# Performance work log

Measured on AMD Instinct MI355X. Metric: run time of the kernel, lower is better.

## Reference

```python
import jax, jax.numpy as jnp
import numpy as np

K_NEIGHBORS = 16
NUM_PATCHES = 32
W_NORMAL = 1.0
W_SURFVAR = 1.0


def _knn_centered(points, k):
    """points: [B, N, 3] -> k nearest neighbors re-centered at each point, [B, N, k, 3].
    Distances are computed on stop_gradient(points) to match torch's .detach()."""
    pd = jax.lax.stop_gradient(points)
    # squared pairwise distances [B, N, N] (sqrt is monotone -> topk order identical)
    d2 = jnp.sum((pd[:, :, None, :] - pd[:, None, :, :]) ** 2, axis=-1)
    _, idx = jax.lax.top_k(-d2, k)  # smallest-k indices, [B, N, k]
    knn = jax.vmap(lambda pts, id_: pts[id_])(points, idx)  # [B, N, k, 3]
    return knn - points[:, :, None, :]


def _eig_props(knn):
    """knn: [B, N, k, 3] -> (normal [B,N,3] = eigvec of smallest eigval, eigvals [B,N,3] ascending)."""
    cov = jnp.einsum('bnki,bnkj->bnij', knn, knn)  # [B, N, 3, 3]
    w, v = jnp.linalg.eigh(cov)  # ascending eigenvalues, matches torch.symeig
    return v[..., :, 0], w


def setup_inputs() -> dict:
    key = jax.random.key(0)
    pointCloud = jax.random.normal(key, (4, 8192, 3), dtype=jnp.float32)
    return {"pointCloud": pointCloud}


def reference(pointCloud):
    B, N, _ = pointCloud.shape
    pp = N // NUM_PATCHES

    # global kNN / normals / surface variance
    knn_g = _knn_centered(pointCloud, K_NEIGHBORS)
    nrm_g, w_g = _eig_props(knn_g)

    # patchwise: each patch is an independent small point cloud -> fold patches into batch
    patch_pts = pointCloud.reshape(B * NUM_PATCHES, pp, 3)
    knn_p = _knn_centered(patch_pts, K_NEIGHBORS)
    nrm_p, w_p = _eig_props(knn_p)
    nrm_p = nrm_p.reshape(B, N, 3)

    # normal loss (abs variant, sign-ambiguity-free)
    loss_n = jnp.mean(jnp.linalg.norm(jnp.abs(nrm_p) - jnp.abs(nrm_g), axis=2)) * W_NORMAL

    # surface variance loss: lambda_min / sum(lambda)
    sv_g = w_g[..., 0] / jnp.sum(w_g, axis=-1)            # [B, N]
    sv_p = (w_p[..., 0] / jnp.sum(w_p, axis=-1)).reshape(B, N)
    loss_sv = jnp.mean((sv_p - sv_g) ** 2) * W_SURFVAR

    return jnp.stack([loss_n, loss_sv])  # [2] (original returns list of two [1] tensors)
```

## Files before the change

### kernel.cpp

```cpp
#include <hip/hip_runtime.h>
#include <math.h>

#define KNN 16
#define NPTS 8192
#define PTCH 256
#define NPATCH 32
#define NBATCH 4
#define NQ 32
#define SSTRIDE 130
#define LAMBDA_T 64.0f

#define NC 16
#define NCELLS (NC * NC * NC)
#define GMIN -4.2f
#define ICS 1.9047619f

__device__ __forceinline__ float lam_f(float r, float s)
{
    const float C     = 0.063493636f;
    const float SQ2PI = 2.5066283f;
    const float IS2   = 0.70710678f;
    float a = fabsf(r - s), b = r + s;
    float amr = a - r;
    float coefA = amr * amr + 2.f - s * s;
    float I = 2.f * __expf(-0.5f * b * b) - coefA * __expf(-0.5f * a * a)
            + r * SQ2PI * (erff(b * IS2) - erff(a * IS2));
    float M = C * (3.14159265f / r) * I;
    if (s > r) {
        float u = s - r;
        M += 12.566371f * C * (1.2533141f * erff(u * IS2) - u * __expf(-0.5f * u * u));
    }
    return (float)NPTS * M;
}

__device__ __forceinline__ void jrot(double& app, double& aqq, double& apq,
                                     double& arp, double& arq,
                                     double& vp0, double& vq0,
                                     double& vp1, double& vq1,
                                     double& vp2, double& vq2)
{
    double g = apq;
    if (g == 0.0) return;
    double theta = (aqq - app) / (2.0 * g);
    double at = fabs(theta);
    double t = (at > 1.0e154) ? (0.5 / theta)
                              : (copysign(1.0, theta) / (at + sqrt(theta * theta + 1.0)));
    double c = 1.0 / sqrt(t * t + 1.0);
    double s = t * c;
    double tau = s / (1.0 + c);
    app -= t * g;
    aqq += t * g;
    apq = 0.0;
    double rp = arp, rq = arq;
    arp = rp - s * (rq + tau * rp);
    arq = rq + s * (rp - tau * rq);
    double p0 = vp0, q0 = vq0;
    vp0 = p0 - s * (q0 + tau * p0); vq0 = q0 + s * (p0 - tau * q0);
    double p1 = vp1, q1 = vq1;
    vp1 = p1 - s * (q1 + tau * p1); vq1 = q1 + s * (p1 - tau * q1);
    double p2 = vp2, q2 = vq2;
    vp2 = p2 - s * (q2 + tau * p2); vq2 = q2 + s * (p2 - tau * q2);
}

__device__ __forceinline__ void eig3(double a00, double a11, double a22,
                                     double a01, double a02, double a12,
                                     double& nx, double& ny, double& nz,
                                     double& lmin, double& lsum)
{
    double v00 = 1, v01 = 0, v02 = 0;
    double v10 = 0, v11 = 1, v12 = 0;
    double v20 = 0, v21 = 0, v22 = 1;
    double scale = fabs(a00) + fabs(a11) + fabs(a22) + fabs(a01) + fabs(a02) + fabs(a12);
    if (scale > 0.0) {
        for (int sweep = 0; sweep < 6; ++sweep) {
            double off = fabs(a01) + fabs(a02) + fabs(a12);
            if (off <= scale * 1e-15) break;
            jrot(a00, a11, a01, a02, a12, v00, v01, v10, v11, v20, v21);
            jrot(a00, a22, a02, a01, a12, v00, v02, v10, v12, v20, v22);
            jrot(a11, a22, a12, a01, a02, v01, v02, v11, v12, v21, v22);
        }
    }
    lsum = a00 + a11 + a22;
    lmin = a00; nx = v00; ny = v10; nz = v20;
    if (a11 < lmin) { lmin = a11; nx = v01; ny = v11; nz = v21; }
    if (a22 < lmin) { lmin = a22; nx = v02; ny = v12; nz = v22; }
}

__device__ __forceinline__ unsigned mkkey(float d2, unsigned idx) {
    return (__float_as_uint(d2) & 0xFFFFE000u) | idx;
}

__device__ __forceinline__ void insert16(unsigned key, unsigned* L)
{
    L[KNN - 1] = key;
    #pragma unroll
    for (int m = KNN - 1; m >= 1; --m) {
        unsigned a = L[m - 1], b = L[m];
        L[m - 1] = min(a, b);
        L[m]     = max(a, b);
    }
}

__device__ __forceinline__ void merge4(unsigned* L, int lane)
{
    #pragma unroll
    for (int step = 1; step <= 2; step <<= 1) {
        unsigned tmp[KNN];
        #pragma unroll
        for (int m = 0; m < KNN; ++m) tmp[m] = __shfl(L[m], lane ^ step, 64);
        for (int m = 0; m < KNN; ++m) {
            if (tmp[m] >= L[KNN - 1]) break;
            insert16(tmp[m], L);
        }
    }
}

__device__ __forceinline__ float rfl(float x) {
    return __int_as_float(__builtin_amdgcn_readfirstlane(__float_as_int(x)));
}
__device__ __forceinline__ unsigned mbcnt64(unsigned long long m) {
    return __builtin_amdgcn_mbcnt_hi((unsigned)(m >> 32),
           __builtin_amdgcn_mbcnt_lo((unsigned)m, 0u));
}

__device__ __forceinline__ int cidx(float v) {
    int i = (int)floorf((v - GMIN) * ICS);
    return min(max(i, 0), NC - 1);
}
__device__ __forceinline__ int cellOf(float x, float y, float z) {
    return (cidx(z) * NC + cidx(y)) * NC + cidx(x);
}

#define BT 1024
__global__ void __launch_bounds__(1024)
build_kernel(const float* __restrict__ pts, float* __restrict__ out,
             unsigned* __restrict__ cellStart, float4* __restrict__ sorted)
{
    __shared__ unsigned hist[NCELLS];
    __shared__ unsigned part[BT];
    const int b = blockIdx.x;
    const int t = threadIdx.x;
    if (b == 0 && t == 0) { out[0] = 0.0f; out[1] = 0.0f; }
    for (int i = t; i < NCELLS; i += BT) hist[i] = 0u;
    __syncthreads();
    const float* base = pts + (size_t)b * (NPTS * 3);
    float px[8], py[8], pz[8];
    int pc[8];
    #pragma unroll
    for (int k = 0; k < 8; ++k) {
        int i = k * BT + t;
        px[k] = base[i * 3 + 0];
        py[k] = base[i * 3 + 1];
        pz[k] = base[i * 3 + 2];
        pc[k] = cellOf(px[k], py[k], pz[k]);
        atomicAdd(&hist[pc[k]], 1u);
    }
    __syncthreads();
    unsigned loc[4], s = 0;
    #pragma unroll
    for (int i = 0; i < 4; ++i) { loc[i] = s; s += hist[t * 4 + i]; }
    part[t] = s;
    __syncthreads();
    for (int o = 1; o < BT; o <<= 1) {
        unsigned u = (t >= o) ? part[t - o] : 0u;
        __syncthreads();
        part[t] += u;
        __syncthreads();
    }
    unsigned basex = part[t] - s;
    unsigned* csb = cellStart + b * (NCELLS + 1);
    #pragma unroll
    for (int i = 0; i < 4; ++i) {
        unsigned e = basex + loc[i];
        csb[t * 4 + i] = e;
        hist[t * 4 + i] = e;
    }
    if (t == BT - 1) csb[NCELLS] = basex + s;
    __syncthreads();
    float4* sb = sorted + (size_t)b * NPTS;
    #pragma unroll
    for (int k = 0; k < 8; ++k) {
        int i = k * BT + t;
        unsigned slot = atomicAdd(&hist[pc[k]], 1u);
        float4 v;
        v.x = px[k]; v.y = py[k]; v.z = pz[k]; v.w = __uint_as_float((unsigned)i);
        sb[slot] = v;
    }
}

__global__ void __launch_bounds__(256, 4)
spl_main(const float* __restrict__ pts, float* __restrict__ out,
         const unsigned* __restrict__ cellStart, const float4* __restrict__ sortedp)
{
    __shared__ float4 pbuf4[PTCH];
    __shared__ unsigned survk[NQ * SSTRIDE];
    __shared__ unsigned cnts[NQ];
    __shared__ float gbuf[NQ];
    __shared__ double xbuf[NQ * 4];
    __shared__ double rb[4];

    const int t = threadIdx.x;
    const int w = t >> 6;
    const int lane = t & 63;
    const int p = blockIdx.x;
    const int eighth = blockIdx.y;
    const int b = blockIdx.z;

    const float* base = pts + (size_t)b * (NPTS * 3);
    const int qbase = p * PTCH + eighth * NQ;
    const unsigned* cs = cellStart + b * (NCELLS + 1);
    const float4* sp = sortedp + (size_t)b * NPTS;

    {
        const float* src = base + p * (PTCH * 3);
        float* dst = (float*)pbuf4;
        #pragma unroll
        for (int s = 0; s < 3; ++s) {
            int f = t + s * 256;
            int j = f / 3;
            int c = f - 3 * j;
            dst[j * 4 + c] = src[f];
        }
    }
    if (t < NQ) {
        int qi = qbase + t;
        float x = base[qi * 3 + 0], y = base[qi * 3 + 1], z = base[qi * 3 + 2];
        float r = fmaxf(sqrtf(x * x + y * y + z * z), 0.01f);
        float lo = 0.f, hi = 12.f;
        #pragma unroll 1
        for (int it = 0; it < 16; ++it) {
            float mid = 0.5f * (lo + hi);
            if (lam_f(r, mid) < LAMBDA_T) lo = mid; else hi = mid;
        }
        gbuf[t] = hi * hi;
    }
    __syncthreads();

    #pragma unroll 1
    for (int u = 0; u < 8; ++u) {
        const int q = w * 8 + u;
        float4 qv = pbuf4[eighth * NQ + q];
        float qx = rfl(qv.x), qy = rfl(qv.y), qz = rfl(qv.z);
        float g2 = rfl(gbuf[q]);
        float g = sqrtf(g2);
        int ixlo = cidx(qx - g), ixhi = cidx(qx + g);
        int iylo = cidx(qy - g), iyhi = cidx(qy + g);
        int izlo = cidx(qz - g), izhi = cidx(qz + g);
        int nx = ixhi - ixlo + 1;
        int ny = iyhi - iylo + 1;
        int nyz = ny * (izhi - izlo + 1);
        const int lR  = (nyz >= 8) ? 3 : (nyz >= 4) ? 2 : (nyz >= 2) ? 1 : 0;
        const int R   = 1 << lR;
        const int lsl = 6 - lR;
        const unsigned SL = 64u >> lR;
        const unsigned slot = (unsigned)lane & (SL - 1u);
        unsigned cnt = 0;
        unsigned sbase = (unsigned)q * SSTRIDE;
        #pragma unroll 1
        for (int r0 = 0; r0 < nyz; r0 += 64) {
            int r = r0 + lane;
            unsigned pk = 0;
            if (r < nyz) {
                int iz = izlo + r / ny;
                int iy = iylo + (r - (r / ny) * ny);
                int cb = (iz * NC + iy) * NC + ixlo;
                unsigned sB = cs[cb];
                pk = sB | ((cs[cb + nx] - sB) << 14);
            }
            int rmax = min(nyz - r0, 64);
            int gcount = (rmax + R - 1) >> lR;
            #pragma unroll 1
            for (int gg = 0; gg < gcount; ++gg) {
                unsigned pkm = __shfl(pk, (gg << lR) + (lane >> lsl), 64);
                unsigned sBm = pkm & 0x3FFFu;
                unsigned lm  = pkm >> 14;
                #pragma unroll 1
                for (unsigned st = slot; ; st += SL) {
                    bool in = st < lm;
                    if (!__any(in ? 1 : 0)) break;
                    float4 c = sp[min(sBm + st, (unsigned)(NPTS - 1))];
                    float dx = qx - c.x, dy = qy - c.y, dz = qz - c.z;
                    float d2 = dx * dx + dy * dy + dz * dz;
                    bool pass = in && (d2 < g2);
                    unsigned long long m = __ballot(pass);
                    if (pass) {
                        unsigned sw = min(cnt + mbcnt64(m), (unsigned)(SSTRIDE - 1));
                        survk[sbase + sw] = mkkey(d2, __float_as_uint(c.w));
                    }
                    cnt += (unsigned)__popcll(m);
                }
            }
        }
        if (lane == 0) cnts[q] = cnt;
    }
    __syncthreads();

    const int qq = lane >> 2;
    const int h = lane & 3;
    const int myq = (w & 1) * 16 + qq;
    float4 qv = pbuf4[eighth * NQ + myq];
    const float pqx = qv.x, pqy = qv.y, pqz = qv.z;

    double ngx = 0, ngy = 0, ngz = 0, svg = 0;

    if (w < 2) {
        unsigned gl[KNN];
        #pragma unroll
        for (int m = 0; m < KNN; ++m) gl[m] = 0xFFFFFFFFu;
        unsigned cnt = cnts[myq];
        bool valid = (cnt >= KNN) && (cnt <= SSTRIDE);
        if (valid) {
            unsigned share = (cnt + 3) >> 2;
            unsigned m0 = h * share;
            unsigned m1 = min(m0 + share, cnt);
            #pragma unroll 1
            for (unsigned m = m0; m < m1; ++m) {
                unsigned k = survk[myq * SSTRIDE + m];
                if (k < gl[KNN - 1]) insert16(k, gl);
            }
        }
        merge4(gl, lane);
        if (valid) {
            float g = gbuf[myq];
            float upper = __uint_as_float((gl[KNN - 1] & 0xFFFFE000u) + 0x2000u);
            valid = (upper < g * 0.999f - 1e-5f);
        }
        if (__any((h == 0 && !valid) ? 1 : 0)) {
            if (h == 0 && !valid) {
                #pragma unroll
                for (int m = 0; m < KNN; ++m) gl[m] = 0xFFFFFFFFu;
                #pragma unroll 1
                for (int i = 0; i < NPTS; ++i) {
                    float cx = base[i * 3 + 0];
                    float cy = base[i * 3 + 1];
                    float cz = base[i * 3 + 2];
                    float dx = pqx - cx, dy = pqy - cy, dz = pqz - cz;
                    float d2 = dx * dx + dy * dy + dz * dz;
                    unsigned k = mkkey(d2, (unsigned)i);
                    if (k < gl[KNN - 1]) insert16(k, gl);
                }
            }
        }
        if (h == 0) {
            double c00 = 0, c11 = 0, c22 = 0, c01 = 0, c02 = 0, c12 = 0;
            const double qxd = pqx, qyd = pqy, qzd = pqz;
            #pragma unroll
            for (int m = 0; m < KNN; ++m) {
                int idx = (int)(gl[m] & 0x1FFFu);
                double dx = (double)base[idx * 3 + 0] - qxd;
                double dy = (double)base[idx * 3 + 1] - qyd;
                double dz = (double)base[idx * 3 + 2] - qzd;
                c00 += dx * dx; c11 += dy * dy; c22 += dz * dz;
                c01 += dx * dy; c02 += dx * dz; c12 += dy * dz;
            }
            double lmin, lsum;
            eig3(c00, c11, c22, c01, c02, c12, ngx, ngy, ngz, lmin, lsum);
            svg = lmin / lsum;
        }
    } else {
        unsigned pl[KNN];
        #pragma unroll
        for (int m = 0; m < KNN; ++m) pl[m] = 0xFFFFFFFFu;
        const int j0 = h * 64;
        #pragma unroll 1
        for (int j = j0; j < j0 + 64; ++j) {
            float4 c = pbuf4[j];
            float dx = pqx - c.x, dy = pqy - c.y, dz = pqz - c.z;
            float d2 = dx * dx + dy * dy + dz * dz;
            unsigned k = mkkey(d2, (unsigned)j);
            if (k < pl[KNN - 1]) insert16(k, pl);
        }
        merge4(pl, lane);
        if (h == 0) {
            double c00 = 0, c11 = 0, c22 = 0, c01 = 0, c02 = 0, c12 = 0;
            const double qxd = pqx, qyd = pqy, qzd = pqz;
            #pragma unroll
            for (int m = 0; m < KNN; ++m) {
                int idx = (int)(pl[m] & 0x1FFFu);
                float4 cpt = pbuf4[idx];
                double dx = (double)cpt.x - qxd;
                double dy = (double)cpt.y - qyd;
                double dz = (double)cpt.z - qzd;
                c00 += dx * dx; c11 += dy * dy; c22 += dz * dz;
                c01 += dx * dy; c02 += dx * dz; c12 += dy * dz;
            }
            double nx, ny, nz, lmin, lsum;
            eig3(c00, c11, c22, c01, c02, c12, nx, ny, nz, lmin, lsum);
            xbuf[myq * 4 + 0] = nx;
            xbuf[myq * 4 + 1] = ny;
            xbuf[myq * 4 + 2] = nz;
            xbuf[myq * 4 + 3] = lmin / lsum;
        }
    }
    __syncthreads();

    double ln = 0.0, lsv = 0.0;
    if (w < 2 && h == 0) {
        double npx = xbuf[myq * 4 + 0];
        double npy = xbuf[myq * 4 + 1];
        double npz = xbuf[myq * 4 + 2];
        double svp = xbuf[myq * 4 + 3];
        double dx = fabs(npx) - fabs(ngx);
        double dy = fabs(npy) - fabs(ngy);
        double dz = fabs(npz) - fabs(ngz);
        ln  = sqrt(dx * dx + dy * dy + dz * dz);
        double ds = svp - svg;
        lsv = ds * ds;
    }
    if (w < 2) {
        #pragma unroll
        for (int o = 32; o > 0; o >>= 1) {
            ln  += __shfl_down(ln, o);
            lsv += __shfl_down(lsv, o);
        }
        if (lane == 0) { rb[w * 2 + 0] = ln; rb[w * 2 + 1] = lsv; }
    }
    __syncthreads();
    if (t == 0) {
        const double inv = 1.0 / (double)(NBATCH * NPTS);
        atomicAdd(&out[0], (float)((rb[0] + rb[2]) * inv));
        atomicAdd(&out[1], (float)((rb[1] + rb[3]) * inv));
    }
}

extern "C" void kernel_launch(void* const* d_in, const int* in_sizes, int n_in,
                              void* d_out, int out_size, void* d_ws, size_t ws_size,
                              hipStream_t stream)
{
    const float* pts = (const float*)d_in[0];
    float* out = (float*)d_out;

    unsigned char* ws = (unsigned char*)d_ws;
    unsigned* cellStart = (unsigned*)(ws);
    float4*   sorted    = (float4*)  (ws + 65552);

    hipLaunchKernelGGL(build_kernel, dim3(NBATCH), dim3(BT), 0, stream,
                       pts, out, cellStart, sorted);
    dim3 grid(NPATCH, 8, NBATCH);
    hipLaunchKernelGGL(spl_main, grid, dim3(256), 0, stream, pts, out, cellStart, sorted);
}
```

Measured before the change: 163.3 us.

## Split fused kNN kernel into gate, filter and select stages via workspace

```diff
diff --git a/kernel.cpp b/kernel.cpp
--- a/kernel.cpp
+++ b/kernel.cpp
@@ -185,6 +185,265 @@
         float4 v;
         v.x = px[k]; v.y = py[k]; v.z = pz[k]; v.w = __uint_as_float((unsigned)i);
         sb[slot] = v;
+    }
+}
+
+__global__ void __launch_bounds__(256)
+gate_kernel(const float* __restrict__ pts, float* __restrict__ g2buf)
+{
+    int q = blockIdx.x * 256 + threadIdx.x;
+    int b = q >> 13, i = q & (NPTS - 1);
+    const float* pp = pts + (size_t)b * (NPTS * 3) + (size_t)i * 3;
+    float x = pp[0], y = pp[1], z = pp[2];
+    float r = fmaxf(sqrtf(x * x + y * y + z * z), 0.01f);
+    float lo = 0.f, hi = 12.f;
+    #pragma unroll 1
+    for (int it = 0; it < 16; ++it) {
+        float mid = 0.5f * (lo + hi);
+        if (lam_f(r, mid) < LAMBDA_T) lo = mid; else hi = mid;
+    }
+    g2buf[q] = hi * hi;
+}
+
+__global__ void __launch_bounds__(256)
+filter_kernel(const float* __restrict__ pts, const float* __restrict__ g2buf,
+              const unsigned* __restrict__ cellStart,
+              const float4* __restrict__ sortedp,
+              unsigned* __restrict__ survk, unsigned* __restrict__ cnts)
+{
+    const int lane = threadIdx.x & 63;
+    const int wq = __builtin_amdgcn_readfirstlane(
+        (int)((blockIdx.x * 256u + (unsigned)threadIdx.x) >> 6));
+    const int b  = wq >> 13;
+    const int qi = wq & (NPTS - 1);
+    const float* base = pts + (size_t)b * (NPTS * 3);
+    const unsigned* cs = cellStart + b * (NCELLS + 1);
+    const float4* sp = sortedp + (size_t)b * NPTS;
+
+    const float qx = base[qi * 3 + 0];
+    const float qy = base[qi * 3 + 1];
+    const float qz = base[qi * 3 + 2];
+    const float g2 = g2buf[wq];
+    const float g  = sqrtf(g2);
+
+    int ixlo = cidx(qx - g), ixhi = cidx(qx + g);
+    int iylo = cidx(qy - g), iyhi = cidx(qy + g);
+    int izlo = cidx(qz - g), izhi = cidx(qz + g);
+    int nx = ixhi - ixlo + 1;
+    int ny = iyhi - iylo + 1;
+    int nyz = ny * (izhi - izlo + 1);
+    const int lR  = (nyz >= 8) ? 3 : (nyz >= 4) ? 2 : (nyz >= 2) ? 1 : 0;
+    const int R   = 1 << lR;
+    const int lsl = 6 - lR;
+    const unsigned SL = 64u >> lR;
+    const unsigned slot = (unsigned)lane & (SL - 1u);
+    unsigned cnt = 0;
+    unsigned sbase = (unsigned)wq * SSTRIDE;
+    #pragma unroll 1
+    for (int r0 = 0; r0 < nyz; r0 += 64) {
+        int r = r0 + lane;
+        unsigned pk = 0;
+        if (r < nyz) {
+            int iz = izlo + r / ny;
+            int iy = iylo + (r - (r / ny) * ny);
+            int cb = (iz * NC + iy) * NC + ixlo;
+            unsigned sB = cs[cb];
+            pk = sB | ((cs[cb + nx] - sB) << 14);
+        }
+        int rmax = min(nyz - r0, 64);
+        int gcount = (rmax + R - 1) >> lR;
+        #pragma unroll 1
+        for (int gg = 0; gg < gcount; ++gg) {
+            unsigned pkm = __shfl(pk, (gg << lR) + (lane >> lsl), 64);
+            unsigned sBm = pkm & 0x3FFFu;
+            unsigned lm  = pkm >> 14;
+            #pragma unroll 1
+            for (unsigned st = slot; ; st += SL) {
+                bool in = st < lm;
+                if (!__any(in ? 1 : 0)) break;
+                float4 c = sp[min(sBm + st, (unsigned)(NPTS - 1))];
+                float dx = qx - c.x, dy = qy - c.y, dz = qz - c.z;
+                float d2 = dx * dx + dy * dy + dz * dz;
+                bool pass = in && (d2 < g2);
+                unsigned long long m = __ballot(pass);
+                if (pass) {
+                    unsigned sw = min(cnt + mbcnt64(m), (unsigned)(SSTRIDE - 1));
+                    survk[sbase + sw] = mkkey(d2, __float_as_uint(c.w));
+                }
+                cnt += (unsigned)__popcll(m);
+            }
+        }
+    }
+    if (lane == 0) cnts[wq] = cnt;
+}
+
+__global__ void __launch_bounds__(256, 4)
+select_kernel(const float* __restrict__ pts, float* __restrict__ out,
+              const float* __restrict__ g2buf,
+              const unsigned* __restrict__ survk_g,
+              const unsigned* __restrict__ cnts_g)
+{
+    __shared__ float4 pbuf4[PTCH];
+    __shared__ unsigned survl[NQ * SSTRIDE];
+    __shared__ unsigned cnts[NQ];
+    __shared__ double xbuf[NQ * 4];
+    __shared__ double rb[4];
+
+    const int t = threadIdx.x;
+    const int w = t >> 6;
+    const int lane = t & 63;
+    const int p = blockIdx.x;
+    const int eighth = blockIdx.y;
+    const int b = blockIdx.z;
+
+    const float* base = pts + (size_t)b * (NPTS * 3);
+    const int qbase = p * PTCH + eighth * NQ;
+    const int qg0 = b * NPTS + qbase;
+
+    {
+        const float* src = base + p * (PTCH * 3);
+        float* dst = (float*)pbuf4;
+        #pragma unroll
+        for (int s = 0; s < 3; ++s) {
+            int f = t + s * 256;
+            int j = f / 3;
+            int c = f - 3 * j;
+            dst[j * 4 + c] = src[f];
+        }
+    }
+    {
+        const unsigned* src = survk_g + (size_t)qg0 * SSTRIDE;
+        #pragma unroll 1
+        for (int i = t; i < NQ * SSTRIDE; i += 256) survl[i] = src[i];
+        if (t < NQ) cnts[t] = cnts_g[qg0 + t];
+    }
+    __syncthreads();
+
+    const int qq = lane >> 2;
+    const int h = lane & 3;
+    const int myq = (w & 1) * 16 + qq;
+    float4 qv = pbuf4[eighth * NQ + myq];
+    const float pqx = qv.x, pqy = qv.y, pqz = qv.z;
+
+    double ngx = 0, ngy = 0, ngz = 0, svg = 0;
+
+    if (w < 2) {
+        unsigned gl[KNN];
+        #pragma unroll
+        for (int m = 0; m < KNN; ++m) gl[m] = 0xFFFFFFFFu;
+        unsigned cnt = cnts[myq];
+        bool valid = (cnt >= KNN) && (cnt <= SSTRIDE);
+        if (valid) {
+            unsigned share = (cnt + 3) >> 2;
+            unsigned m0 = h * share;
+            unsigned m1 = min(m0 + share, cnt);
+            #pragma unroll 1
+            for (unsigned m = m0; m < m1; ++m) {
+                unsigned k = survl[myq * SSTRIDE + m];
+                if (k < gl[KNN - 1]) insert16(k, gl);
+            }
+        }
+        merge4(gl, lane);
+        if (valid) {
+            float g = g2buf[qg0 + myq];
+            float upper = __uint_as_float((gl[KNN - 1] & 0xFFFFE000u) + 0x2000u);
+            valid = (upper < g * 0.999f - 1e-5f);
+        }
+        if (__any((h == 0 && !valid) ? 1 : 0)) {
+            if (h == 0 && !valid) {
+                #pragma unroll
+                for (int m = 0; m < KNN; ++m) gl[m] = 0xFFFFFFFFu;
+                #pragma unroll 1
+                for (int i = 0; i < NPTS; ++i) {
+                    float cx = base[i * 3 + 0];
+                    float cy = base[i * 3 + 1];
+                    float cz = base[i * 3 + 2];
+                    float dx = pqx - cx, dy = pqy - cy, dz = pqz - cz;
+                    float d2 = dx * dx + dy * dy + dz * dz;
+                    unsigned k = mkkey(d2, (unsigned)i);
+                    if (k < gl[KNN - 1]) insert16(k, gl);
+                }
+            }
+        }
+        if (h == 0) {
+            double c00 = 0, c11 = 0, c22 = 0, c01 = 0, c02 = 0, c12 = 0;
+            const double qxd = pqx, qyd = pqy, qzd = pqz;
+            #pragma unroll
+            for (int m = 0; m < KNN; ++m) {
+                int idx = (int)(gl[m] & 0x1FFFu);
+                double dx = (double)base[idx * 3 + 0] - qxd;
+                double dy = (double)base[idx * 3 + 1] - qyd;
+                double dz = (double)base[idx * 3 + 2] - qzd;
+                c00 += dx * dx; c11 += dy * dy; c22 += dz * dz;
+                c01 += dx * dy; c02 += dx * dz; c12 += dy * dz;
+            }
+            double lmin, lsum;
+            eig3(c00, c11, c22, c01, c02, c12, ngx, ngy, ngz, lmin, lsum);
+            svg = lmin / lsum;
+        }
+    } else {
+        unsigned pl[KNN];
+        #pragma unroll
+        for (int m = 0; m < KNN; ++m) pl[m] = 0xFFFFFFFFu;
+        const int j0 = h * 64;
+        #pragma unroll 1
+        for (int j = j0; j < j0 + 64; ++j) {
+            float4 c = pbuf4[j];
+            float dx = pqx - c.x, dy = pqy - c.y, dz = pqz - c.z;
+            float d2 = dx * dx + dy * dy + dz * dz;
+            unsigned k = mkkey(d2, (unsigned)j);
+            if (k < pl[KNN - 1]) insert16(k, pl);
+        }
+        merge4(pl, lane);
+        if (h == 0) {
+            double c00 = 0, c11 = 0, c22 = 0, c01 = 0, c02 = 0, c12 = 0;
+            const double qxd = pqx, qyd = pqy, qzd = pqz;
+            #pragma unroll
+            for (int m = 0; m < KNN; ++m) {
+                int idx = (int)(pl[m] & 0x1FFFu);
+                float4 cpt = pbuf4[idx];
+                double dx = (double)cpt.x - qxd;
+                double dy = (double)cpt.y - qyd;
+                double dz = (double)cpt.z - qzd;
+                c00 += dx * dx; c11 += dy * dy; c22 += dz * dz;
+                c01 += dx * dy; c02 += dx * dz; c12 += dy * dz;
+            }
+            double nx, ny, nz, lmin, lsum;
+            eig3(c00, c11, c22, c01, c02, c12, nx, ny, nz, lmin, lsum);
+            xbuf[myq * 4 + 0] = nx;
+            xbuf[myq * 4 + 1] = ny;
+            xbuf[myq * 4 + 2] = nz;
+            xbuf[myq * 4 + 3] = lmin / lsum;
+        }
+    }
+    __syncthreads();
+
+    double ln = 0.0, lsv = 0.0;
+    if (w < 2 && h == 0) {
+        double npx = xbuf[myq * 4 + 0];
+        double npy = xbuf[myq * 4 + 1];
+        double npz = xbuf[myq * 4 + 2];
+        double svp = xbuf[myq * 4 + 3];
+        double dx = fabs(npx) - fabs(ngx);
+        double dy = fabs(npy) - fabs(ngy);
+        double dz = fabs(npz) - fabs(ngz);
+        ln  = sqrt(dx * dx + dy * dy + dz * dz);
+        double ds = svp - svg;
+        lsv = ds * ds;
+    }
+    if (w < 2) {
+        #pragma unroll
+        for (int o = 32; o > 0; o >>= 1) {
+            ln  += __shfl_down(ln, o);
+            lsv += __shfl_down(lsv, o);
+        }
+        if (lane == 0) { rb[w * 2 + 0] = ln; rb[w * 2 + 1] = lsv; }
+    }
+    __syncthreads();
+    if (t == 0) {
+        const double inv = 1.0 / (double)(NBATCH * NPTS);
+        atomicAdd(&out[0], (float)((rb[0] + rb[2]) * inv));
+        atomicAdd(&out[1], (float)((rb[1] + rb[3]) * inv));
     }
 }
 
@@ -433,9 +692,23 @@
     unsigned char* ws = (unsigned char*)d_ws;
     unsigned* cellStart = (unsigned*)(ws);
     float4*   sorted    = (float4*)  (ws + 65552);
+    float*    g2buf     = (float*)   (ws + 589840);
+    unsigned* cnts      = (unsigned*)(ws + 720912);
+    unsigned* survk     = (unsigned*)(ws + 851984);
 
     hipLaunchKernelGGL(build_kernel, dim3(NBATCH), dim3(BT), 0, stream,
                        pts, out, cellStart, sorted);
-    dim3 grid(NPATCH, 8, NBATCH);
-    hipLaunchKernelGGL(spl_main, grid, dim3(256), 0, stream, pts, out, cellStart, sorted);
-}
+    if (ws_size >= (size_t)17891344) {
+        hipLaunchKernelGGL(gate_kernel, dim3(NBATCH * NPTS / 256), dim3(256), 0, stream,
+                           pts, g2buf);
+        hipLaunchKernelGGL(filter_kernel, dim3(NBATCH * NPTS / 4), dim3(256), 0, stream,
+                           pts, g2buf, cellStart, sorted, survk, cnts);
+        dim3 grid(NPATCH, 8, NBATCH);
+        hipLaunchKernelGGL(select_kernel, grid, dim3(256), 0, stream,
+                           pts, out, g2buf, survk, cnts);
+    } else {
+        dim3 grid(NPATCH, 8, NBATCH);
+        hipLaunchKernelGGL(spl_main, grid, dim3(256), 0, stream,
+                           pts, out, cellStart, sorted);
+    }
+}
```

Result: no change. 162.1 us (-0.7%).

## Split fused kNN kernel into gate, select, patch-select, eigen and reduce stages

Applied to the files above, without the earlier changes.

```diff
diff --git a/kernel.cpp b/kernel.cpp
--- a/kernel.cpp
+++ b/kernel.cpp
@@ -6,7 +6,6 @@
 #define PTCH 256
 #define NPATCH 32
 #define NBATCH 4
-#define NQ 32
 #define SSTRIDE 130
 #define LAMBDA_T 64.0f
 
@@ -115,9 +114,6 @@
     }
 }
 
-__device__ __forceinline__ float rfl(float x) {
-    return __int_as_float(__builtin_amdgcn_readfirstlane(__float_as_int(x)));
-}
 __device__ __forceinline__ unsigned mbcnt64(unsigned long long m) {
     return __builtin_amdgcn_mbcnt_hi((unsigned)(m >> 32),
            __builtin_amdgcn_mbcnt_lo((unsigned)m, 0u));
@@ -188,28 +184,159 @@
     }
 }
 
-__global__ void __launch_bounds__(256, 4)
-spl_main(const float* __restrict__ pts, float* __restrict__ out,
-         const unsigned* __restrict__ cellStart, const float4* __restrict__ sortedp)
+__global__ void __launch_bounds__(256)
+gate_kernel(const float* __restrict__ pts, float* __restrict__ g2buf)
+{
+    int q = blockIdx.x * 256 + threadIdx.x;
+    int b = q >> 13, i = q & (NPTS - 1);
+    const float* pp = pts + (size_t)b * (NPTS * 3) + (size_t)i * 3;
+    float x = pp[0], y = pp[1], z = pp[2];
+    float r = fmaxf(sqrtf(x * x + y * y + z * z), 0.01f);
+    float lo = 0.f, hi = 12.f;
+    #pragma unroll 1
+    for (int it = 0; it < 16; ++it) {
+        float mid = 0.5f * (lo + hi);
+        if (lam_f(r, mid) < LAMBDA_T) lo = mid; else hi = mid;
+    }
+    g2buf[q] = hi * hi;
+}
+
+__global__ void __launch_bounds__(256)
+fselect_kernel(const float* __restrict__ pts, const float* __restrict__ g2buf,
+               const unsigned* __restrict__ cellStart,
+               const float4* __restrict__ sortedp,
+               unsigned* __restrict__ idx16)
+{
+    __shared__ unsigned survl[4 * SSTRIDE];
+    const int t = threadIdx.x;
+    const int wv = t >> 6;
+    const int lane = t & 63;
+    const int wq = __builtin_amdgcn_readfirstlane(blockIdx.x * 4 + wv);
+    const int b  = wq >> 13;
+    const int qi = wq & (NPTS - 1);
+    const float* base = pts + (size_t)b * (NPTS * 3);
+    const unsigned* cs = cellStart + b * (NCELLS + 1);
+    const float4* sp = sortedp + (size_t)b * NPTS;
+    unsigned* sl = survl + wv * SSTRIDE;
+
+    const float qx = base[qi * 3 + 0];
+    const float qy = base[qi * 3 + 1];
+    const float qz = base[qi * 3 + 2];
+    const float g2 = g2buf[wq];
+    const float g  = sqrtf(g2);
+
+    int ixlo = cidx(qx - g), ixhi = cidx(qx + g);
+    int iylo = cidx(qy - g), iyhi = cidx(qy + g);
+    int izlo = cidx(qz - g), izhi = cidx(qz + g);
+    int nx = ixhi - ixlo + 1;
+    int ny = iyhi - iylo + 1;
+    int nyz = ny * (izhi - izlo + 1);
+    const int lR  = (nyz >= 8) ? 3 : (nyz >= 4) ? 2 : (nyz >= 2) ? 1 : 0;
+    const int R   = 1 << lR;
+    const int lsl = 6 - lR;
+    const unsigned SL = 64u >> lR;
+    const unsigned slot = (unsigned)lane & (SL - 1u);
+    unsigned cnt = 0;
+    #pragma unroll 1
+    for (int r0 = 0; r0 < nyz; r0 += 64) {
+        int r = r0 + lane;
+        unsigned pk = 0;
+        if (r < nyz) {
+            int iz = izlo + r / ny;
+            int iy = iylo + (r - (r / ny) * ny);
+            int cb = (iz * NC + iy) * NC + ixlo;
+            unsigned sB = cs[cb];
+            pk = sB | ((cs[cb + nx] - sB) << 14);
+        }
+        int rmax = min(nyz - r0, 64);
+        int gcount = (rmax + R - 1) >> lR;
+        #pragma unroll 1
+        for (int gg = 0; gg < gcount; ++gg) {
+            unsigned pkm = __shfl(pk, (gg << lR) + (lane >> lsl), 64);
+            unsigned sBm = pkm & 0x3FFFu;
+            unsigned lm  = pkm >> 14;
+            #pragma unroll 1
+            for (unsigned st = slot; ; st += SL) {
+                bool in = st < lm;
+                if (!__any(in ? 1 : 0)) break;
+                float4 c = sp[min(sBm + st, (unsigned)(NPTS - 1))];
+                float dx = qx - c.x, dy = qy - c.y, dz = qz - c.z;
+                float d2 = dx * dx + dy * dy + dz * dz;
+                bool pass = in && (d2 < g2);
+                unsigned long long m = __ballot(pass);
+                if (pass) {
+                    unsigned sw = min(cnt + mbcnt64(m), (unsigned)(SSTRIDE - 1));
+                    sl[sw] = mkkey(d2, __float_as_uint(c.w));
+                }
+                cnt += (unsigned)__popcll(m);
+            }
+        }
+    }
+
+    bool valid = (cnt >= KNN) && (cnt <= 128u);
+    if (valid) {
+        unsigned k0 = (lane < (int)cnt)      ? sl[lane]      : 0xFFFFFFFFu;
+        unsigned k1 = (lane + 64 < (int)cnt) ? sl[lane + 64] : 0xFFFFFFFFu;
+        unsigned P = 0;
+        #pragma unroll 1
+        for (int bit = 31; bit >= 0; --bit) {
+            unsigned mid = P | (1u << bit);
+            unsigned c = (unsigned)__popcll(__ballot(k0 < mid))
+                       + (unsigned)__popcll(__ballot(k1 < mid));
+            if (c < 16u) P = mid;
+        }
+        float upper = __uint_as_float((P & 0xFFFFE000u) + 0x2000u);
+        valid = (upper < g2 * 0.999f - 1e-5f);
+        if (valid) {
+            bool sel0 = (k0 <= P);
+            bool sel1 = (k1 <= P);
+            unsigned long long m0 = __ballot(sel0);
+            unsigned long long m1 = __ballot(sel1);
+            unsigned base1 = (unsigned)__popcll(m0);
+            if (sel0) sl[mbcnt64(m0)] = k0;
+            if (sel1) sl[base1 + mbcnt64(m1)] = k1;
+            unsigned myk = sl[lane & 15];
+            unsigned rnk = 0;
+            #pragma unroll
+            for (int j = 0; j < 16; ++j) {
+                unsigned kj = __shfl(myk, j, 64);
+                rnk += (kj < myk) ? 1u : 0u;
+            }
+            if (lane < 16)
+                idx16[(size_t)wq * 32 + rnk] = myk & 0x1FFFu;
+        }
+    }
+    if (!valid && lane == 0) {
+        unsigned gl[KNN];
+        #pragma unroll
+        for (int m = 0; m < KNN; ++m) gl[m] = 0xFFFFFFFFu;
+        #pragma unroll 1
+        for (int i = 0; i < NPTS; ++i) {
+            float cx = base[i * 3 + 0];
+            float cy = base[i * 3 + 1];
+            float cz = base[i * 3 + 2];
+            float dx = qx - cx, dy = qy - cy, dz = qz - cz;
+            float d2 = dx * dx + dy * dy + dz * dz;
+            unsigned k = mkkey(d2, (unsigned)i);
+            if (k < gl[KNN - 1]) insert16(k, gl);
+        }
+        unsigned* dst = idx16 + (size_t)wq * 32;
+        #pragma unroll
+        for (int m = 0; m < KNN; ++m) dst[m] = gl[m] & 0x1FFFu;
+    }
+}
+
+__global__ void __launch_bounds__(256)
+pselect_kernel(const float* __restrict__ pts, unsigned* __restrict__ idx16)
 {
     __shared__ float4 pbuf4[PTCH];
-    __shared__ unsigned survk[NQ * SSTRIDE];
-    __shared__ unsigned cnts[NQ];
-    __shared__ float gbuf[NQ];
-    __shared__ double xbuf[NQ * 4];
-    __shared__ double rb[4];
-
     const int t = threadIdx.x;
     const int w = t >> 6;
     const int lane = t & 63;
     const int p = blockIdx.x;
-    const int eighth = blockIdx.y;
+    const int quarter = blockIdx.y;
     const int b = blockIdx.z;
-
     const float* base = pts + (size_t)b * (NPTS * 3);
-    const int qbase = p * PTCH + eighth * NQ;
-    const unsigned* cs = cellStart + b * (NCELLS + 1);
-    const float4* sp = sortedp + (size_t)b * NPTS;
 
     {
         const float* src = base + p * (PTCH * 3);
@@ -222,204 +349,114 @@
             dst[j * 4 + c] = src[f];
         }
     }
-    if (t < NQ) {
-        int qi = qbase + t;
-        float x = base[qi * 3 + 0], y = base[qi * 3 + 1], z = base[qi * 3 + 2];
-        float r = fmaxf(sqrtf(x * x + y * y + z * z), 0.01f);
-        float lo = 0.f, hi = 12.f;
-        #pragma unroll 1
-        for (int it = 0; it < 16; ++it) {
-            float mid = 0.5f * (lo + hi);
-            if (lam_f(r, mid) < LAMBDA_T) lo = mid; else hi = mid;
-        }
-        gbuf[t] = hi * hi;
-    }
-    __syncthreads();
-
-    #pragma unroll 1
-    for (int u = 0; u < 8; ++u) {
-        const int q = w * 8 + u;
-        float4 qv = pbuf4[eighth * NQ + q];
-        float qx = rfl(qv.x), qy = rfl(qv.y), qz = rfl(qv.z);
-        float g2 = rfl(gbuf[q]);
-        float g = sqrtf(g2);
-        int ixlo = cidx(qx - g), ixhi = cidx(qx + g);
-        int iylo = cidx(qy - g), iyhi = cidx(qy + g);
-        int izlo = cidx(qz - g), izhi = cidx(qz + g);
-        int nx = ixhi - ixlo + 1;
-        int ny = iyhi - iylo + 1;
-        int nyz = ny * (izhi - izlo + 1);
-        const int lR  = (nyz >= 8) ? 3 : (nyz >= 4) ? 2 : (nyz >= 2) ? 1 : 0;
-        const int R   = 1 << lR;
-        const int lsl = 6 - lR;
-        const unsigned SL = 64u >> lR;
-        const unsigned slot = (unsigned)lane & (SL - 1u);
-        unsigned cnt = 0;
-        unsigned sbase = (unsigned)q * SSTRIDE;
-        #pragma unroll 1
-        for (int r0 = 0; r0 < nyz; r0 += 64) {
-            int r = r0 + lane;
-            unsigned pk = 0;
-            if (r < nyz) {
-                int iz = izlo + r / ny;
-                int iy = iylo + (r - (r / ny) * ny);
-                int cb = (iz * NC + iy) * NC + ixlo;
-                unsigned sB = cs[cb];
-                pk = sB | ((cs[cb + nx] - sB) << 14);
-            }
-            int rmax = min(nyz - r0, 64);
-            int gcount = (rmax + R - 1) >> lR;
-            #pragma unroll 1
-            for (int gg = 0; gg < gcount; ++gg) {
-                unsigned pkm = __shfl(pk, (gg << lR) + (lane >> lsl), 64);
-                unsigned sBm = pkm & 0x3FFFu;
-                unsigned lm  = pkm >> 14;
-                #pragma unroll 1
-                for (unsigned st = slot; ; st += SL) {
-                    bool in = st < lm;
-                    if (!__any(in ? 1 : 0)) break;
-                    float4 c = sp[min(sBm + st, (unsigned)(NPTS - 1))];
-                    float dx = qx - c.x, dy = qy - c.y, dz = qz - c.z;
-                    float d2 = dx * dx + dy * dy + dz * dz;
-                    bool pass = in && (d2 < g2);
-                    unsigned long long m = __ballot(pass);
-                    if (pass) {
-                        unsigned sw = min(cnt + mbcnt64(m), (unsigned)(SSTRIDE - 1));
-                        survk[sbase + sw] = mkkey(d2, __float_as_uint(c.w));
-                    }
-                    cnt += (unsigned)__popcll(m);
-                }
-            }
-        }
-        if (lane == 0) cnts[q] = cnt;
-    }
     __syncthreads();
 
     const int qq = lane >> 2;
     const int h = lane & 3;
-    const int myq = (w & 1) * 16 + qq;
-    float4 qv = pbuf4[eighth * NQ + myq];
+    const int qlocal = quarter * 64 + w * 16 + qq;
+    float4 qv = pbuf4[qlocal];
     const float pqx = qv.x, pqy = qv.y, pqz = qv.z;
 
-    double ngx = 0, ngy = 0, ngz = 0, svg = 0;
-
-    if (w < 2) {
-        unsigned gl[KNN];
+    unsigned pl[KNN];
+    #pragma unroll
+    for (int m = 0; m < KNN; ++m) pl[m] = 0xFFFFFFFFu;
+    const int j0 = h * 64;
+    #pragma unroll 4
+    for (int j = j0; j < j0 + 64; ++j) {
+        float4 c = pbuf4[j];
+        float dx = pqx - c.x, dy = pqy - c.y, dz = pqz - c.z;
+        float d2 = dx * dx + dy * dy + dz * dz;
+        unsigned k = mkkey(d2, (unsigned)j);
+        if (k < pl[KNN - 1]) insert16(k, pl);
+    }
+    merge4(pl, lane);
+    if (h == 0) {
+        int qid = b * NPTS + p * PTCH + qlocal;
+        unsigned* dst = idx16 + (size_t)qid * 32 + 16;
         #pragma unroll
-        for (int m = 0; m < KNN; ++m) gl[m] = 0xFFFFFFFFu;
-        unsigned cnt = cnts[myq];
-        bool valid = (cnt >= KNN) && (cnt <= SSTRIDE);
-        if (valid) {
-            unsigned share = (cnt + 3) >> 2;
-            unsigned m0 = h * share;
-            unsigned m1 = min(m0 + share, cnt);
-            #pragma unroll 1
-            for (unsigned m = m0; m < m1; ++m) {
-                unsigned k = survk[myq * SSTRIDE + m];
-                if (k < gl[KNN - 1]) insert16(k, gl);
-            }
-        }
-        merge4(gl, lane);
-        if (valid) {
-            float g = gbuf[myq];
-            float upper = __uint_as_float((gl[KNN - 1] & 0xFFFFE000u) + 0x2000u);
-            valid = (upper < g * 0.999f - 1e-5f);
-        }
-        if (__any((h == 0 && !valid) ? 1 : 0)) {
-            if (h == 0 && !valid) {
-                #pragma unroll
-                for (int m = 0; m < KNN; ++m) gl[m] = 0xFFFFFFFFu;
-                #pragma unroll 1
-                for (int i = 0; i < NPTS; ++i) {
-                    float cx = base[i * 3 + 0];
-                    float cy = base[i * 3 + 1];
-                    float cz = base[i * 3 + 2];
-                    float dx = pqx - cx, dy = pqy - cy, dz = pqz - cz;
-                    float d2 = dx * dx + dy * dy + dz * dz;
-                    unsigned k = mkkey(d2, (unsigned)i);
-                    if (k < gl[KNN - 1]) insert16(k, gl);
-                }
-            }
-        }
-        if (h == 0) {
-            double c00 = 0, c11 = 0, c22 = 0, c01 = 0, c02 = 0, c12 = 0;
-            const double qxd = pqx, qyd = pqy, qzd = pqz;
-            #pragma unroll
-            for (int m = 0; m < KNN; ++m) {
-                int idx = (int)(gl[m] & 0x1FFFu);
-                double dx = (double)base[idx * 3 + 0] - qxd;
-                double dy = (double)base[idx * 3 + 1] - qyd;
-                double dz = (double)base[idx * 3 + 2] - qzd;
-                c00 += dx * dx; c11 += dy * dy; c22 += dz * dz;
-                c01 += dx * dy; c02 += dx * dz; c12 += dy * dz;
-            }
-            double lmin, lsum;
-            eig3(c00, c11, c22, c01, c02, c12, ngx, ngy, ngz, lmin, lsum);
-            svg = lmin / lsum;
-        }
-    } else {
-        unsigned pl[KNN];
-        #pragma unroll
-        for (int m = 0; m < KNN; ++m) pl[m] = 0xFFFFFFFFu;
-        const int j0 = h * 64;
-        #pragma unroll 1
-        for (int j = j0; j < j0 + 64; ++j) {
-            float4 c = pbuf4[j];
-            float dx = pqx - c.x, dy = pqy - c.y, dz = pqz - c.z;
-            float d2 = dx * dx + dy * dy + dz * dz;
-            unsigned k = mkkey(d2, (unsigned)j);
-            if (k < pl[KNN - 1]) insert16(k, pl);
-        }
-        merge4(pl, lane);
-        if (h == 0) {
-            double c00 = 0, c11 = 0, c22 = 0, c01 = 0, c02 = 0, c12 = 0;
-            const double qxd = pqx, qyd = pqy, qzd = pqz;
-            #pragma unroll
-            for (int m = 0; m < KNN; ++m) {
-                int idx = (int)(pl[m] & 0x1FFFu);
-                float4 cpt = pbuf4[idx];
-                double dx = (double)cpt.x - qxd;
-                double dy = (double)cpt.y - qyd;
-                double dz = (double)cpt.z - qzd;
-                c00 += dx * dx; c11 += dy * dy; c22 += dz * dz;
-                c01 += dx * dy; c02 += dx * dz; c12 += dy * dz;
-            }
-            double nx, ny, nz, lmin, lsum;
-            eig3(c00, c11, c22, c01, c02, c12, nx, ny, nz, lmin, lsum);
-            xbuf[myq * 4 + 0] = nx;
-            xbuf[myq * 4 + 1] = ny;
-            xbuf[myq * 4 + 2] = nz;
-            xbuf[myq * 4 + 3] = lmin / lsum;
-        }
-    }
-    __syncthreads();
+        for (int m = 0; m < KNN; ++m)
+            dst[m] = (unsigned)(p * PTCH) + (pl[m] & 0x1FFFu);
+    }
+}
+
+__global__ void __launch_bounds__(256)
+eig_loss_kernel(const float* __restrict__ pts,
+                const unsigned* __restrict__ idx16,
+                double* __restrict__ partials)
+{
+    __shared__ double sln[4], slv[4];
+    const int t = threadIdx.x;
+    const int e = blockIdx.x * 256 + t;
+    const int qid = e >> 1;
+    const int b = qid >> 13;
+    const int qi = qid & (NPTS - 1);
+    const float* base = pts + (size_t)b * (NPTS * 3);
+
+    const double qxd = (double)base[qi * 3 + 0];
+    const double qyd = (double)base[qi * 3 + 1];
+    const double qzd = (double)base[qi * 3 + 2];
+
+    const unsigned* L = idx16 + (size_t)qid * 32 + (e & 1) * 16;
+    double c00 = 0, c11 = 0, c22 = 0, c01 = 0, c02 = 0, c12 = 0;
+    #pragma unroll
+    for (int m = 0; m < KNN; ++m) {
+        int idx = (int)L[m];
+        double dx = (double)base[idx * 3 + 0] - qxd;
+        double dy = (double)base[idx * 3 + 1] - qyd;
+        double dz = (double)base[idx * 3 + 2] - qzd;
+        c00 += dx * dx; c11 += dy * dy; c22 += dz * dz;
+        c01 += dx * dy; c02 += dx * dz; c12 += dy * dz;
+    }
+    double nx, ny, nz, lmin, lsum;
+    eig3(c00, c11, c22, c01, c02, c12, nx, ny, nz, lmin, lsum);
+    double sv = lmin / lsum;
+
+    double onx = __shfl_xor(nx, 1, 64);
+    double ony = __shfl_xor(ny, 1, 64);
+    double onz = __shfl_xor(nz, 1, 64);
+    double osv = __shfl_xor(sv, 1, 64);
 
     double ln = 0.0, lsv = 0.0;
-    if (w < 2 && h == 0) {
-        double npx = xbuf[myq * 4 + 0];
-        double npy = xbuf[myq * 4 + 1];
-        double npz = xbuf[myq * 4 + 2];
-        double svp = xbuf[myq * 4 + 3];
-        double dx = fabs(npx) - fabs(ngx);
-        double dy = fabs(npy) - fabs(ngy);
-        double dz = fabs(npz) - fabs(ngz);
+    if ((e & 1) == 0) {
+        double dx = fabs(onx) - fabs(nx);
+        double dy = fabs(ony) - fabs(ny);
+        double dz = fabs(onz) - fabs(nz);
         ln  = sqrt(dx * dx + dy * dy + dz * dz);
-        double ds = svp - svg;
+        double ds = osv - sv;
         lsv = ds * ds;
     }
-    if (w < 2) {
-        #pragma unroll
-        for (int o = 32; o > 0; o >>= 1) {
-            ln  += __shfl_down(ln, o);
-            lsv += __shfl_down(lsv, o);
-        }
-        if (lane == 0) { rb[w * 2 + 0] = ln; rb[w * 2 + 1] = lsv; }
-    }
+    #pragma unroll
+    for (int o = 32; o > 0; o >>= 1) {
+        ln  += __shfl_down(ln, o);
+        lsv += __shfl_down(lsv, o);
+    }
+    const int w = t >> 6;
+    if ((t & 63) == 0) { sln[w] = ln; slv[w] = lsv; }
+    __syncthreads();
+    if (t == 0) {
+        partials[blockIdx.x * 2 + 0] = sln[0] + sln[1] + sln[2] + sln[3];
+        partials[blockIdx.x * 2 + 1] = slv[0] + slv[1] + slv[2] + slv[3];
+    }
+}
+
+__global__ void __launch_bounds__(256)
+reduce_kernel(const double* __restrict__ partials, float* __restrict__ out)
+{
+    __shared__ double sln[4], slv[4];
+    const int t = threadIdx.x;
+    double a = partials[t * 2 + 0];
+    double c = partials[t * 2 + 1];
+    #pragma unroll
+    for (int o = 32; o > 0; o >>= 1) {
+        a += __shfl_down(a, o);
+        c += __shfl_down(c, o);
+    }
+    if ((t & 63) == 0) { sln[t >> 6] = a; slv[t >> 6] = c; }
     __syncthreads();
     if (t == 0) {
         const double inv = 1.0 / (double)(NBATCH * NPTS);
-        atomicAdd(&out[0], (float)((rb[0] + rb[2]) * inv));
-        atomicAdd(&out[1], (float)((rb[1] + rb[3]) * inv));
+        out[0] = (float)((sln[0] + sln[1] + sln[2] + sln[3]) * inv);
+        out[1] = (float)((slv[0] + slv[1] + slv[2] + slv[3]) * inv);
     }
 }
 
@@ -433,9 +470,20 @@
     unsigned char* ws = (unsigned char*)d_ws;
     unsigned* cellStart = (unsigned*)(ws);
     float4*   sorted    = (float4*)  (ws + 65552);
+    float*    g2buf     = (float*)   (ws + 589840);
+    unsigned* idx16     = (unsigned*)(ws + 720912);
+    double*   partials  = (double*)  (ws + 4915216);
 
     hipLaunchKernelGGL(build_kernel, dim3(NBATCH), dim3(BT), 0, stream,
                        pts, out, cellStart, sorted);
-    dim3 grid(NPATCH, 8, NBATCH);
-    hipLaunchKernelGGL(spl_main, grid, dim3(256), 0, stream, pts, out, cellStart, sorted);
-}
+    hipLaunchKernelGGL(gate_kernel, dim3(NBATCH * NPTS / 256), dim3(256), 0, stream,
+                       pts, g2buf);
+    hipLaunchKernelGGL(fselect_kernel, dim3(NBATCH * NPTS / 4), dim3(256), 0, stream,
+                       pts, g2buf, cellStart, sorted, idx16);
+    hipLaunchKernelGGL(pselect_kernel, dim3(NPATCH, 4, NBATCH), dim3(256), 0, stream,
+                       pts, idx16);
+    hipLaunchKernelGGL(eig_loss_kernel, dim3(NBATCH * NPTS * 2 / 256), dim3(256),
+                       0, stream, pts, idx16, partials);
+    hipLaunchKernelGGL(reduce_kernel, dim3(1), dim3(256), 0, stream,
+                       partials, out);
+}
```

Result: faster. 151.4 us (-7.2%).
